# Optimization experiments

Hardware: AMD Instinct MI355X
Metric: run time of the kernel (lower is better)

The kernel has to match this reference:

```python
import jax, jax.numpy as jnp
import numpy as np

N_HEADS = 16
LN_EPS = 1e-6


def _mha(q_in, kv_in, mask, wq, bq, wk, bk, wv, bv, wo, bo):
    B, Sq, D = q_in.shape
    H = N_HEADS
    dh = D // H
    def split(x):  # [B,S,D] -> [B,H,S,dh]
        return x.reshape(B, -1, H, dh).transpose(0, 2, 1, 3)
    q = split(q_in @ wq + bq)
    k = split(kv_in @ wk + bk)
    v = split(kv_in @ wv + bv)
    scores = jnp.einsum('bhqd,bhkd->bhqk', q, k) / jnp.sqrt(jnp.asarray(dh, q.dtype))
    scores = scores + mask * (-1e9)
    attn = jax.nn.softmax(scores, axis=-1)
    out = jnp.einsum('bhqk,bhkd->bhqd', attn, v)
    out = out.transpose(0, 2, 1, 3).reshape(B, Sq, D)
    return out @ wo + bo


def _layer_norm(x, gamma, beta):
    mu = jnp.mean(x, axis=-1, keepdims=True)
    var = jnp.mean(jnp.square(x - mu), axis=-1, keepdims=True)
    return (x - mu) * jax.lax.rsqrt(var + LN_EPS) * gamma + beta


def setup_inputs() -> dict:
    key = jax.random.key(0)
    B, S_dec, S_enc, D, F = 4, 1024, 1024, 1024, 4096
    ks = jax.random.split(key, 16)
    s = 0.02
    inp = {
        'inputs': jax.random.normal(ks[0], (B, S_dec, D), jnp.float32),
        'enc_outputs': jax.random.normal(ks[1], (B, S_enc, D), jnp.float32),
        # causal look-ahead mask: 1 above diagonal -> -1e9 added to scores
        'mask_1': jnp.triu(jnp.ones((S_dec, S_dec), jnp.float32), k=1)[None, None],
        'mask_2': jnp.zeros((B, 1, 1, S_enc), jnp.float32),
    }
    names = ['wq1', 'wk1', 'wv1', 'wo1', 'wq2', 'wk2', 'wv2', 'wo2']
    for i, n in enumerate(names):
        inp[n] = jax.random.normal(ks[2 + i], (D, D), jnp.float32) * s
        inp['b' + n[1:]] = jnp.zeros((D,), jnp.float32)
    inp['w_ff1'] = jax.random.normal(ks[10], (D, F), jnp.float32) * s
    inp['b_ff1'] = jnp.zeros((F,), jnp.float32)
    inp['w_ff2'] = jax.random.normal(ks[11], (F, D), jnp.float32) * s
    inp['b_ff2'] = jnp.zeros((D,), jnp.float32)
    for i in (1, 2, 3):
        inp[f'g{i}'] = jnp.ones((D,), jnp.float32)
        inp[f'beta{i}'] = jnp.zeros((D,), jnp.float32)
    return inp


def reference(inputs, enc_outputs, mask_1, mask_2,
              wq1, bq1, wk1, bk1, wv1, bv1, wo1, bo1,
              wq2, bq2, wk2, bk2, wv2, bv2, wo2, bo2,
              w_ff1, b_ff1, w_ff2, b_ff2,
              g1, beta1, g2, beta2, g3, beta3):
    # causal self-attention + residual + LN (dropout inactive at inference)
    attn = _mha(inputs, inputs, mask_1, wq1, bq1, wk1, bk1, wv1, bv1, wo1, bo1)
    attn = _layer_norm(attn + inputs, g1, beta1)
    # encoder-decoder cross-attention + residual + LN
    attn2 = _mha(attn, enc_outputs, mask_2, wq2, bq2, wk2, bk2, wv2, bv2, wo2, bo2)
    attn2 = _layer_norm(attn2 + attn, g2, beta2)
    # FFN + residual + LN
    h = jax.nn.relu(attn2 @ w_ff1 + b_ff1)
    h = h @ w_ff2 + b_ff2
    return _layer_norm(h + attn2, g3, beta3)
```

## Files before the change

### kernel.cpp

```cpp
#include <hip/hip_runtime.h>
#include <stdint.h>

typedef unsigned short ushort_t;
typedef __attribute__((ext_vector_type(8))) short bf16x8;
typedef __attribute__((ext_vector_type(4))) float f32x4;
typedef __attribute__((ext_vector_type(4))) unsigned short us4;

#define DEV __device__ __forceinline__

DEV unsigned short f2bf(float f) {
  union { float f; unsigned u; } x; x.f = f;
  unsigned r = x.u + 0x7fffu + ((x.u >> 16) & 1u);
  return (unsigned short)(r >> 16);
}

DEV float bf2f(unsigned short u) {
  union { unsigned u; float f; } x; x.u = (unsigned)u << 16; return x.f;
}

DEV uint2 pk4(float v0, float v1, float v2, float v3) {
  unsigned d0, d1;
  asm("v_cvt_pk_bf16_f32 %0, %1, %2" : "=v"(d0) : "v"(v0), "v"(v1));
  asm("v_cvt_pk_bf16_f32 %0, %1, %2" : "=v"(d1) : "v"(v2), "v"(v3));
  uint2 r; r.x = d0; r.y = d1; return r;
}

DEV void gload16(const void* g, void* l) {
  __builtin_amdgcn_global_load_lds(
      (const __attribute__((address_space(1))) unsigned int*)g,
      (__attribute__((address_space(3))) unsigned int*)l, 16, 0, 0);
}

#define MFMA16 __builtin_amdgcn_mfma_f32_16x16x32_bf16

__global__ __launch_bounds__(256) void cast2_bf16_kernel(
    const float* __restrict__ x0, ushort_t* __restrict__ y0,
    const float* __restrict__ x1, ushort_t* __restrict__ y1) {
  int blk = blockIdx.x;
  const float* x = (blk < 4096) ? x0 : x1;
  ushort_t* y = (blk < 4096) ? y0 : y1;
  int i = (blk & 4095) * 256 + threadIdx.x;
  float4 v = ((const float4*)x)[i];
  us4 o; o.x = f2bf(v.x); o.y = f2bf(v.y); o.z = f2bf(v.z); o.w = f2bf(v.w);
  ((us4*)y)[i] = o;
}

__global__ __launch_bounds__(256) void reduce_cast_kernel(
    const ushort_t* __restrict__ p0, const ushort_t* __restrict__ p1,
    ushort_t* __restrict__ y, int n4) {
  int i = blockIdx.x * 256 + threadIdx.x;
  if (i >= n4) return;
  us4 a = ((const us4*)p0)[i];
  us4 b = ((const us4*)p1)[i];
  us4 o;
  o.x = f2bf(bf2f(a.x) + bf2f(b.x));
  o.y = f2bf(bf2f(a.y) + bf2f(b.y));
  o.z = f2bf(bf2f(a.z) + bf2f(b.z));
  o.w = f2bf(bf2f(a.w) + bf2f(b.w));
  ((us4*)y)[i] = o;
}

__global__ __launch_bounds__(256) void transpose_cast_kernel(
    const float* __restrict__ W, ushort_t* __restrict__ dst, int K, int N) {
  __shared__ float tile[64][65];
  int n0 = blockIdx.x * 64, k0 = blockIdx.y * 64;
  int tid = threadIdx.x;
#pragma unroll
  for (int it = 0; it < 16; ++it) {
    int idx = it * 256 + tid; int r = idx >> 6, c = idx & 63;
    tile[r][c] = W[(size_t)(k0 + r) * N + n0 + c];
  }
  __syncthreads();
#pragma unroll
  for (int it = 0; it < 16; ++it) {
    int idx = it * 256 + tid; int r = idx >> 6, c = idx & 63;
    dst[(size_t)(n0 + r) * K + k0 + c] = f2bf(tile[c][r]);
  }
}

struct Src8 { const float* p[8]; };
__global__ __launch_bounds__(256) void transpose_cast8_kernel(
    Src8 s, ushort_t* __restrict__ dst) {
  __shared__ float tile[64][65];
  const float* W = s.p[blockIdx.z];
  ushort_t* out = dst + (size_t)blockIdx.z * 1048576;
  int n0 = blockIdx.x * 64, k0 = blockIdx.y * 64;
  int tid = threadIdx.x;
#pragma unroll
  for (int it = 0; it < 16; ++it) {
    int idx = it * 256 + tid; int r = idx >> 6, c = idx & 63;
    tile[r][c] = W[(size_t)(k0 + r) * 1024 + n0 + c];
  }
  __syncthreads();
#pragma unroll
  for (int it = 0; it < 16; ++it) {
    int idx = it * 256 + tid; int r = idx >> 6, c = idx & 63;
    out[(size_t)(n0 + r) * 1024 + k0 + c] = f2bf(tile[c][r]);
  }
}

__global__ __launch_bounds__(256) void transpose_v_kernel(
    const ushort_t* __restrict__ V, int ldv, ushort_t* __restrict__ vT) {
  __shared__ ushort_t tile[64][65];
  int s0 = blockIdx.x * 64;
  int bh = blockIdx.y;
  int b = bh >> 4, h = bh & 15;
  int tid = threadIdx.x;
#pragma unroll
  for (int it = 0; it < 4; ++it) {
    int idx = it * 256 + tid; int r = idx >> 4, c = (idx & 15) * 4;
    us4 v = *(const us4*)&V[(size_t)(b * 1024 + s0 + r) * ldv + h * 64 + c];
    tile[r][c] = v.x; tile[r][c + 1] = v.y; tile[r][c + 2] = v.z; tile[r][c + 3] = v.w;
  }
  __syncthreads();
#pragma unroll
  for (int it = 0; it < 4; ++it) {
    int idx = it * 256 + tid; int r = idx >> 4, c = (idx & 15) * 4;
    us4 o; o.x = tile[c][r]; o.y = tile[c + 1][r]; o.z = tile[c + 2][r]; o.w = tile[c + 3][r];
    *(us4*)&vT[((size_t)bh * 64 + r) * 1024 + s0 + c] = o;
  }
}

template <int RELU>
__global__ __launch_bounds__(256, 2) void gemm_bt(
    const ushort_t* __restrict__ A, const ushort_t* __restrict__ Bt,
    const float* __restrict__ b0, const float* __restrict__ b1,
    const float* __restrict__ b2, const float* __restrict__ b3,
    ushort_t* __restrict__ Cb, int M, int N, int K, int Ks, long long pstr) {
  __shared__ ushort_t sA[4096];
  __shared__ ushort_t sB[4096];
  const int tid = threadIdx.x;
  const int w = tid >> 6, lane = tid & 63;
  const int lrow = lane & 15, lk = lane >> 4;
  const int m0 = blockIdx.x * 128, n0 = blockIdx.y * 128;
  const int kz = blockIdx.z * Ks;
  const int wr = w >> 1, wc = w & 1;
  f32x4 acc[4][4] = {};
  const int brow0 = (w * 1024 + lane * 16) >> 6;
  const int kbyte = (lane * 16) & 63;

  for (int kt = kz; kt < kz + Ks; kt += 32) {
    __syncthreads();
    const ushort_t* ga = A + (size_t)(m0 + brow0) * K + kt + (kbyte >> 1);
    gload16(ga, (char*)sA + w * 1024);
    gload16(ga + (size_t)64 * K, (char*)sA + 4096 + w * 1024);
    const ushort_t* gb = Bt + (size_t)(n0 + brow0) * K + kt + (kbyte >> 1);
    gload16(gb, (char*)sB + w * 1024);
    gload16(gb + (size_t)64 * K, (char*)sB + 4096 + w * 1024);
    __syncthreads();
    bf16x8 aF[4], bF[4];
#pragma unroll
    for (int t = 0; t < 4; ++t) {
      bF[t] = *(const bf16x8*)((const char*)sB + ((wc * 64 + t * 16 + lrow) << 6) + (lk << 4));
      aF[t] = *(const bf16x8*)((const char*)sA + ((wr * 64 + t * 16 + lrow) << 6) + (lk << 4));
    }
#pragma unroll
    for (int mt = 0; mt < 4; ++mt)
#pragma unroll
      for (int nt = 0; nt < 4; ++nt)
        acc[mt][nt] = MFMA16(bF[nt], aF[mt], acc[mt][nt], 0, 0, 0);
  }
  ushort_t* Cbz = Cb + (long long)blockIdx.z * pstr;
#pragma unroll
  for (int nt = 0; nt < 4; ++nt) {
    int colb = n0 + wc * 64 + nt * 16 + lk * 4;
    int seg = colb >> 10;
    const float* bp = seg == 0 ? b0 : seg == 1 ? b1 : seg == 2 ? b2 : b3;
    float4 bv = *(const float4*)(bp + (colb & 1023));
    if (blockIdx.z != 0) { bv.x = bv.y = bv.z = bv.w = 0.f; }
#pragma unroll
    for (int mt = 0; mt < 4; ++mt) {
      int row = m0 + wr * 64 + mt * 16 + lrow;
      float v0 = acc[mt][nt][0] + bv.x, v1 = acc[mt][nt][1] + bv.y;
      float v2 = acc[mt][nt][2] + bv.z, v3 = acc[mt][nt][3] + bv.w;
      if (RELU) {
        v0 = fmaxf(v0, 0.f); v1 = fmaxf(v1, 0.f);
        v2 = fmaxf(v2, 0.f); v3 = fmaxf(v3, 0.f);
      }
      *(uint2*)&Cbz[(size_t)row * N + colb] = pk4(v0, v1, v2, v3);
    }
  }
}

template <int RELU>
__global__ __launch_bounds__(512, 1) void gemm256(
    const ushort_t* __restrict__ A, const ushort_t* __restrict__ Bt,
    const float* __restrict__ b0, const float* __restrict__ b1,
    const float* __restrict__ b2, const float* __restrict__ b3,
    ushort_t* __restrict__ Cb, int M, int N, int K, int Ks, long long pstr) {
  extern __shared__ char L[];
  const int tid = threadIdx.x;
  const int w = tid >> 6, lane = tid & 63;
  const int lrow = lane & 15, lk = lane >> 4;
  const int wm = w >> 2, wn = w & 3;
  const int m0 = blockIdx.x * 256, n0 = blockIdx.y * 256;
  const int kz = blockIdx.z * Ks;
  const int nt = Ks >> 6;

  const int srow = w * 8 + (lane >> 3);
  const int gsw = (lane & 7) ^ ((lane >> 3) & 7);
  const ushort_t* srcA = A + (size_t)(m0 + srow) * K + kz + gsw * 8;
  const ushort_t* srcB = Bt + (size_t)(n0 + srow) * K + kz + gsw * 8;
  const int dstw = w * 1024;

#define STG4(M_, T_)                                                  \
  do {                                                                \
    const ushort_t* g0 = ((M_) ? srcB : srcA) + (size_t)(T_) * 64;    \
    char* d_ = L + (((T_) & 1) << 16) + ((M_) << 15) + dstw;          \
    gload16(g0, d_);                                                  \
    gload16(g0 + (size_t)64 * K, d_ + 8192);                          \
    gload16(g0 + (size_t)128 * K, d_ + 16384);                        \
    gload16(g0 + (size_t)192 * K, d_ + 24576);                        \
  } while (0)

  f32x4 acc[8][4] = {};
  const int swz = (lrow & 7) << 4;
  const int k0b = (lk << 4) ^ swz;
  const int k1b = (64 + (lk << 4)) ^ swz;
  const int aBase = (wm * 128 + lrow) << 7;
  const int bBase = ((wn * 64 + lrow) << 7) + 32768;

  STG4(0, 0); STG4(1, 0);
  asm volatile("s_waitcnt vmcnt(0)" ::: "memory");
  __builtin_amdgcn_s_barrier();

  for (int t = 0; t < nt; ++t) {
    const char* base = L + ((t & 1) << 16);
    bf16x8 aF[8], bF[4];
    if (t + 1 < nt) STG4(1, t + 1);
#pragma unroll
    for (int n = 0; n < 4; ++n) bF[n] = *(const bf16x8*)(base + bBase + n * 2048 + k0b);
#pragma unroll
    for (int m = 0; m < 8; ++m) aF[m] = *(const bf16x8*)(base + aBase + m * 2048 + k0b);
    __builtin_amdgcn_s_setprio(1);
#pragma unroll
    for (int m = 0; m < 8; ++m)
#pragma unroll
      for (int n = 0; n < 4; ++n)
        acc[m][n] = MFMA16(bF[n], aF[m], acc[m][n], 0, 0, 0);
    __builtin_amdgcn_s_setprio(0);
    if (t + 1 < nt) STG4(0, t + 1);
#pragma unroll
    for (int n = 0; n < 4; ++n) bF[n] = *(const bf16x8*)(base + bBase + n * 2048 + k1b);
#pragma unroll
    for (int m = 0; m < 8; ++m) aF[m] = *(const bf16x8*)(base + aBase + m * 2048 + k1b);
    __builtin_amdgcn_s_setprio(1);
#pragma unroll
    for (int m = 0; m < 8; ++m)
#pragma unroll
      for (int n = 0; n < 4; ++n)
        acc[m][n] = MFMA16(bF[n], aF[m], acc[m][n], 0, 0, 0);
    __builtin_amdgcn_s_setprio(0);
    asm volatile("s_waitcnt lgkmcnt(0)" ::: "memory");
    asm volatile("s_waitcnt vmcnt(0)" ::: "memory");
    __builtin_amdgcn_s_barrier();
  }
#undef STG4

  ushort_t* Cbz = Cb + (long long)blockIdx.z * pstr;
#pragma unroll
  for (int n = 0; n < 4; ++n) {
    int colb = n0 + wn * 64 + n * 16 + lk * 4;
    int seg = colb >> 10;
    const float* bp = seg == 0 ? b0 : seg == 1 ? b1 : seg == 2 ? b2 : b3;
    float4 bv = *(const float4*)(bp + (colb & 1023));
    if (blockIdx.z != 0) { bv.x = bv.y = bv.z = bv.w = 0.f; }
#pragma unroll
    for (int m = 0; m < 8; ++m) {
      int row = m0 + wm * 128 + m * 16 + lrow;
      float v0 = acc[m][n][0] + bv.x, v1 = acc[m][n][1] + bv.y;
      float v2 = acc[m][n][2] + bv.z, v3 = acc[m][n][3] + bv.w;
      if (RELU) {
        v0 = fmaxf(v0, 0.f); v1 = fmaxf(v1, 0.f);
        v2 = fmaxf(v2, 0.f); v3 = fmaxf(v3, 0.f);
      }
      *(uint2*)&Cbz[(size_t)row * N + colb] = pk4(v0, v1, v2, v3);
    }
  }
}

template <int CAUSAL>
__global__ __launch_bounds__(256, 3) void attn_kernel(
    const ushort_t* __restrict__ Q, int ldq,
    const ushort_t* __restrict__ Kp, int ldk,
    const ushort_t* __restrict__ vT,
    const float* __restrict__ mask2,
    ushort_t* __restrict__ O) {
  __shared__ ushort_t sK[2][4096];
  __shared__ ushort_t sV[2][4096];
  __shared__ ushort_t sP[4][2048];
  const int bh = blockIdx.x;
  const int yb = blockIdx.y;
  const int qb = (yb < 4) ? yb : 11 - yb;
  const int b = bh >> 4, h = bh & 15;
  const int tid = threadIdx.x, w = tid >> 6, lane = tid & 63;
  const int lrow = lane & 15, lk = lane >> 4;
  const int q0 = qb * 128 + w * 32;

  bf16x8 qF[2][2];
#pragma unroll
  for (int g = 0; g < 2; ++g) {
    const ushort_t* qptr =
        Q + (size_t)(b * 1024 + q0 + g * 16 + lrow) * ldq + h * 64 + lk * 8;
    qF[g][0] = *(const bf16x8*)qptr;
    qF[g][1] = *(const bf16x8*)(qptr + 32);
  }
  f32x4 oacc[2][4] = {};
  float m_[2] = {-3.0e38f, -3.0e38f}, l_[2] = {0.f, 0.f};
  const int nkb = CAUSAL ? (qb * 2 + 2) : 16;
  const float C = 0.18033688011112042f;

  const int sr = w * 16 + (lane >> 3);
  const int scb = (((lane & 7) ^ (lane >> 3)) * 16);
  const ushort_t* kbase = Kp + (size_t)(b * 1024 + sr) * ldk + h * 64 + (scb >> 1);
  const ushort_t* vbase = vT + ((size_t)bh * 64 + sr) * 1024 + (scb >> 1);
  char* dstK0 = (char*)sK[0] + w * 2048;
  char* dstV0 = (char*)sV[0] + w * 2048;

#define STAGE(kb_, bufi)                                              \
  do {                                                                \
    const ushort_t* gk = kbase + (size_t)(kb_) * 64 * ldk;            \
    gload16(gk, dstK0 + (bufi) * 8192);                               \
    gload16(gk + (size_t)8 * ldk, dstK0 + (bufi) * 8192 + 1024);      \
    const ushort_t* gv = vbase + (kb_) * 64;                          \
    gload16(gv, dstV0 + (bufi) * 8192);                               \
    gload16(gv + (size_t)8 * 1024, dstV0 + (bufi) * 8192 + 1024);     \
  } while (0)

  STAGE(0, 0);
  const int swz = (lrow & 7) << 4;

  for (int kb = 0; kb < nkb; ++kb) {
    const int buf = kb & 1;
    __syncthreads();
    if (kb + 1 < nkb) STAGE(kb + 1, buf ^ 1);

    const char* kB = (const char*)sK[buf];
    const char* vB = (const char*)sV[buf];
    bool skip[2], edge[2];
#pragma unroll
    for (int g = 0; g < 2; ++g) {
      int qming = q0 + g * 16;
      skip[g] = CAUSAL && (kb * 64 > qming + 15);
      edge[g] = CAUSAL && !skip[g] && (kb * 64 + 63 > qming);
    }
    f32x4 sc[2][4];
    __builtin_amdgcn_s_setprio(1);
#pragma unroll
    for (int kt = 0; kt < 4; ++kt) {
      const char* rp = kB + ((kt * 16 + lrow) << 7);
      bf16x8 k0 = *(const bf16x8*)(rp + ((lk * 16) ^ swz));
      bf16x8 k1 = *(const bf16x8*)(rp + ((64 + lk * 16) ^ swz));
      f32x4 z0 = {};
      z0 = MFMA16(k0, qF[0][0], z0, 0, 0, 0);
      sc[0][kt] = MFMA16(k1, qF[0][1], z0, 0, 0, 0);
      f32x4 z1 = {};
      z1 = MFMA16(k0, qF[1][0], z1, 0, 0, 0);
      sc[1][kt] = MFMA16(k1, qF[1][1], z1, 0, 0, 0);
    }
    __builtin_amdgcn_s_setprio(0);
    float4 mv[4];
    if (!CAUSAL) {
#pragma unroll
      for (int kt = 0; kt < 4; ++kt)
        mv[kt] = *(const float4*)&mask2[b * 1024 + kb * 64 + kt * 16 + lk * 4];
    }
#pragma unroll
    for (int g = 0; g < 2; ++g) {
      if (skip[g]) continue;
      if (CAUSAL) {
        if (edge[g]) {
          int qrel = q0 + g * 16 + lrow - kb * 64;
#pragma unroll
          for (int kt = 0; kt < 4; ++kt)
#pragma unroll
            for (int j = 0; j < 4; ++j)
              if (kt * 16 + lk * 4 + j > qrel) sc[g][kt][j] = -3.0e38f;
        }
      } else {
#pragma unroll
        for (int kt = 0; kt < 4; ++kt) {
          sc[g][kt][0] = fmaf(mv[kt].x, -8e9f, sc[g][kt][0]);
          sc[g][kt][1] = fmaf(mv[kt].y, -8e9f, sc[g][kt][1]);
          sc[g][kt][2] = fmaf(mv[kt].z, -8e9f, sc[g][kt][2]);
          sc[g][kt][3] = fmaf(mv[kt].w, -8e9f, sc[g][kt][3]);
        }
      }
      float a0 = fmaxf(fmaxf(sc[g][0][0], sc[g][0][1]), sc[g][0][2]);
      float a1 = fmaxf(fmaxf(sc[g][0][3], sc[g][1][0]), sc[g][1][1]);
      float a2 = fmaxf(fmaxf(sc[g][1][2], sc[g][1][3]), sc[g][2][0]);
      float a3 = fmaxf(fmaxf(sc[g][2][1], sc[g][2][2]), sc[g][2][3]);
      float a4 = fmaxf(fmaxf(sc[g][3][0], sc[g][3][1]), sc[g][3][2]);
      float pmax = fmaxf(fmaxf(fmaxf(a0, a1), fmaxf(a2, a3)),
                         fmaxf(a4, sc[g][3][3]));
      pmax = fmaxf(pmax, __shfl_xor(pmax, 16));
      pmax = fmaxf(pmax, __shfl_xor(pmax, 32));
      if (__any(pmax - m_[g] > 64.f)) {
        float mnew = fmaxf(m_[g], pmax);
        float scale = __builtin_exp2f((m_[g] - mnew) * C);
        l_[g] *= scale;
        m_[g] = mnew;
#pragma unroll
        for (int t = 0; t < 4; ++t) {
          oacc[g][t][0] *= scale; oacc[g][t][1] *= scale;
          oacc[g][t][2] *= scale; oacc[g][t][3] *= scale;
        }
      }
      const float mC = m_[g] * C;
      float psk[4] = {0.f, 0.f, 0.f, 0.f};
#pragma unroll
      for (int kt = 0; kt < 4; ++kt)
#pragma unroll
        for (int j = 0; j < 4; ++j) {
          float e = __builtin_exp2f(fmaf(sc[g][kt][j], C, -mC));
          sc[g][kt][j] = e;
          psk[kt] += e;
        }
      float ps = (psk[0] + psk[1]) + (psk[2] + psk[3]);
      ps += __shfl_xor(ps, 16);
      ps += __shfl_xor(ps, 32);
      l_[g] += ps;
      char* bp = (char*)sP[w] + (g * 16 + lrow) * 128;
#pragma unroll
      for (int kt = 0; kt < 4; ++kt) {
        uint2 dd = pk4(sc[g][kt][0], sc[g][kt][1], sc[g][kt][2], sc[g][kt][3]);
        *(uint2*)(bp + ((kt * 32 + lk * 8) ^ swz)) = dd;
      }
    }
    bf16x8 pF[2][2];
#pragma unroll
    for (int g = 0; g < 2; ++g) {
      if (skip[g]) continue;
      const char* pB = (const char*)sP[w] + (g * 16 + lrow) * 128;
      pF[g][0] = *(const bf16x8*)(pB + ((lk * 16) ^ swz));
      pF[g][1] = *(const bf16x8*)(pB + ((64 + lk * 16) ^ swz));
    }
    __builtin_amdgcn_s_setprio(1);
#pragma unroll
    for (int t = 0; t < 4; ++t) {
      const char* rp = vB + ((t * 16 + lrow) << 7);
      bf16x8 v0 = *(const bf16x8*)(rp + ((lk * 16) ^ swz));
      bf16x8 v1 = *(const bf16x8*)(rp + ((64 + lk * 16) ^ swz));
      if (!skip[0]) {
        oacc[0][t] = MFMA16(v0, pF[0][0], oacc[0][t], 0, 0, 0);
        oacc[0][t] = MFMA16(v1, pF[0][1], oacc[0][t], 0, 0, 0);
      }
      if (!skip[1]) {
        oacc[1][t] = MFMA16(v0, pF[1][0], oacc[1][t], 0, 0, 0);
        oacc[1][t] = MFMA16(v1, pF[1][1], oacc[1][t], 0, 0, 0);
      }
    }
    __builtin_amdgcn_s_setprio(0);
  }
#undef STAGE
#pragma unroll
  for (int g = 0; g < 2; ++g) {
    float invl = 1.f / l_[g];
    int row = q0 + g * 16 + lrow;
    ushort_t* op = O + (size_t)(b * 1024 + row) * 1024 + h * 64;
#pragma unroll
    for (int t = 0; t < 4; ++t) {
      uint2 dd = pk4(oacc[g][t][0] * invl, oacc[g][t][1] * invl,
                     oacc[g][t][2] * invl, oacc[g][t][3] * invl);
      *(uint2*)&op[t * 16 + lk * 4] = dd;
    }
  }
}

template <int RESBF, int NPART, int WF32>
__global__ __launch_bounds__(256) void ln_kernel(
    const ushort_t* __restrict__ p0, const ushort_t* __restrict__ p1,
    const ushort_t* __restrict__ p2, const ushort_t* __restrict__ p3,
    const void* __restrict__ rp,
    const float* __restrict__ g, const float* __restrict__ be,
    float* __restrict__ yf, ushort_t* __restrict__ yb) {
  int row = blockIdx.x, tid = threadIdx.x;
  size_t off = (size_t)row * 1024 + tid * 4;
  us4 a = *(const us4*)(p0 + off);
  float x0 = bf2f(a.x), x1 = bf2f(a.y), x2 = bf2f(a.z), x3 = bf2f(a.w);
  if (NPART >= 2) {
    us4 t = *(const us4*)(p1 + off);
    x0 += bf2f(t.x); x1 += bf2f(t.y); x2 += bf2f(t.z); x3 += bf2f(t.w);
  }
  if (NPART >= 4) {
    us4 t2 = *(const us4*)(p2 + off);
    us4 t3 = *(const us4*)(p3 + off);
    x0 += bf2f(t2.x) + bf2f(t3.x); x1 += bf2f(t2.y) + bf2f(t3.y);
    x2 += bf2f(t2.z) + bf2f(t3.z); x3 += bf2f(t2.w) + bf2f(t3.w);
  }
  if (RESBF) {
    us4 r = *(const us4*)((const ushort_t*)rp + off);
    x0 += bf2f(r.x); x1 += bf2f(r.y); x2 += bf2f(r.z); x3 += bf2f(r.w);
  } else {
    float4 r = *(const float4*)((const float*)rp + off);
    x0 += r.x; x1 += r.y; x2 += r.z; x3 += r.w;
  }
  float s = x0 + x1 + x2 + x3;
  float s2 = x0 * x0 + x1 * x1 + x2 * x2 + x3 * x3;
#pragma unroll
  for (int o = 1; o < 64; o <<= 1) { s += __shfl_xor(s, o); s2 += __shfl_xor(s2, o); }
  __shared__ float sh[8];
  if ((tid & 63) == 0) { sh[tid >> 6] = s; sh[4 + (tid >> 6)] = s2; }
  __syncthreads();
  s = sh[0] + sh[1] + sh[2] + sh[3];
  s2 = sh[4] + sh[5] + sh[6] + sh[7];
  float mu = s * 0.0009765625f;
  float var = s2 * 0.0009765625f - mu * mu;
  float inv = rsqrtf(var + 1e-6f);
  float4 gv = *(const float4*)(g + tid * 4);
  float4 bv = *(const float4*)(be + tid * 4);
  float y0 = (x0 - mu) * inv * gv.x + bv.x;
  float y1 = (x1 - mu) * inv * gv.y + bv.y;
  float y2 = (x2 - mu) * inv * gv.z + bv.z;
  float y3 = (x3 - mu) * inv * gv.w + bv.w;
  if (WF32) {
    *(float4*)(yf + off) = make_float4(y0, y1, y2, y3);
  } else {
    us4 o; o.x = f2bf(y0); o.y = f2bf(y1); o.z = f2bf(y2); o.w = f2bf(y3);
    *(us4*)(yb + off) = o;
  }
}

extern "C" void kernel_launch(void* const* d_in, const int* in_sizes, int n_in,
                              void* d_out, int out_size, void* d_ws, size_t ws_size,
                              hipStream_t stream) {
  (void)in_sizes; (void)n_in; (void)out_size; (void)ws_size;
  const float* inputs = (const float*)d_in[0];
  const float* enc    = (const float*)d_in[1];
  const float* mask2  = (const float*)d_in[3];
  const float* wq1 = (const float*)d_in[4];  const float* bq1 = (const float*)d_in[5];
  const float* wk1 = (const float*)d_in[6];  const float* bk1 = (const float*)d_in[7];
  const float* wv1 = (const float*)d_in[8];  const float* bv1 = (const float*)d_in[9];
  const float* wo1 = (const float*)d_in[10]; const float* bo1 = (const float*)d_in[11];
  const float* wq2 = (const float*)d_in[12]; const float* bq2 = (const float*)d_in[13];
  const float* wk2 = (const float*)d_in[14]; const float* bk2 = (const float*)d_in[15];
  const float* wv2 = (const float*)d_in[16]; const float* bv2 = (const float*)d_in[17];
  const float* wo2 = (const float*)d_in[18]; const float* bo2 = (const float*)d_in[19];
  const float* wff1 = (const float*)d_in[20]; const float* bff1 = (const float*)d_in[21];
  const float* wff2 = (const float*)d_in[22]; const float* bff2 = (const float*)d_in[23];
  const float* g1 = (const float*)d_in[24]; const float* be1 = (const float*)d_in[25];
  const float* g2 = (const float*)d_in[26]; const float* be2 = (const float*)d_in[27];
  const float* g3 = (const float*)d_in[28]; const float* be3 = (const float*)d_in[29];

  char* ws = (char*)d_ws;
  const size_t MB = 1024 * 1024;
  const size_t W1M = 1048576;
  ushort_t* wt    = (ushort_t*)ws;
  ushort_t* xb    = (ushort_t*)(ws + 32 * MB);
  ushort_t* encb  = (ushort_t*)(ws + 40 * MB);
  ushort_t* qkvb  = (ushort_t*)(ws + 48 * MB);
  ushort_t* vtb   = (ushort_t*)(ws + 72 * MB);
  ushort_t* attnb = (ushort_t*)(ws + 80 * MB);
  ushort_t* y1b   = (ushort_t*)(ws + 88 * MB);
  ushort_t* y2b   = (ushort_t*)(ws + 96 * MB);
  ushort_t* cp    = (ushort_t*)(ws + 104 * MB);
  ushort_t* q2b   = (ushort_t*)(ws + 32 * MB);
  ushort_t* kv2b  = (ushort_t*)(ws + 56 * MB);
  ushort_t* hb    = (ushort_t*)(ws + 32 * MB);
  ushort_t* pp    = (ushort_t*)(ws + 104 * MB);
  float* outf = (float*)d_out;
  const long long PE = 4LL * 1024 * 1024;

  cast2_bf16_kernel<<<8192, 256, 0, stream>>>(inputs, xb, enc, encb);
  Src8 s8; s8.p[0] = wq1; s8.p[1] = wk1; s8.p[2] = wv1; s8.p[3] = wo1;
           s8.p[4] = wq2; s8.p[5] = wk2; s8.p[6] = wv2; s8.p[7] = wo2;
  transpose_cast8_kernel<<<dim3(16, 16, 8), 256, 0, stream>>>(s8, wt);
  transpose_cast_kernel<<<dim3(64, 16), 256, 0, stream>>>(wff1, wt + 8 * W1M, 1024, 4096);
  transpose_cast_kernel<<<dim3(16, 64), 256, 0, stream>>>(wff2, wt + 12 * W1M, 4096, 1024);

  gemm256<0><<<dim3(16, 12, 1), 512, 131072, stream>>>(
      xb, wt, bq1, bk1, bv1, bv1, qkvb, 4096, 3072, 1024, 1024, 0);
  transpose_v_kernel<<<dim3(16, 64), 256, 0, stream>>>(qkvb + 2048, 3072, vtb);
  attn_kernel<1><<<dim3(64, 8), 256, 0, stream>>>(
      qkvb, 3072, qkvb + 1024, 3072, vtb, nullptr, attnb);
  gemm_bt<0><<<dim3(32, 8, 2), 256, 0, stream>>>(
      attnb, wt + 3 * W1M, bo1, bo1, bo1, bo1, cp, 4096, 1024, 1024, 512, PE);
  ln_kernel<0, 2, 0><<<4096, 256, 0, stream>>>(cp, cp + PE, nullptr, nullptr,
                                               inputs, g1, be1, nullptr, y1b);

  gemm_bt<0><<<dim3(32, 8, 2), 256, 0, stream>>>(
      y1b, wt + 4 * W1M, bq2, bq2, bq2, bq2, cp, 4096, 1024, 1024, 512, PE);
  reduce_cast_kernel<<<4096, 256, 0, stream>>>(cp, cp + PE, q2b, 1048576);
  gemm_bt<0><<<dim3(32, 16, 1), 256, 0, stream>>>(
      encb, wt + 5 * W1M, bk2, bv2, bk2, bk2, kv2b, 4096, 2048, 1024, 1024, 0);
  transpose_v_kernel<<<dim3(16, 64), 256, 0, stream>>>(kv2b + 1024, 2048, vtb);
  attn_kernel<0><<<dim3(64, 8), 256, 0, stream>>>(
      q2b, 1024, kv2b, 2048, vtb, mask2, attnb);
  gemm_bt<0><<<dim3(32, 8, 2), 256, 0, stream>>>(
      attnb, wt + 7 * W1M, bo2, bo2, bo2, bo2, cp, 4096, 1024, 1024, 512, PE);
  ln_kernel<1, 2, 0><<<4096, 256, 0, stream>>>(cp, cp + PE, nullptr, nullptr,
                                               y1b, g2, be2, nullptr, y2b);

  gemm256<1><<<dim3(16, 16, 1), 512, 131072, stream>>>(
      y2b, wt + 8 * W1M, bff1, bff1 + 1024, bff1 + 2048, bff1 + 3072,
      hb, 4096, 4096, 1024, 1024, 0);
  gemm256<0><<<dim3(16, 4, 4), 512, 131072, stream>>>(
      hb, wt + 12 * W1M, bff2, bff2, bff2, bff2, pp, 4096, 1024, 4096, 1024, PE);
  ln_kernel<1, 4, 1><<<4096, 256, 0, stream>>>(pp, pp + PE, pp + 2 * PE, pp + 3 * PE,
                                               y2b, g3, be3, outf, nullptr);
}
```

Baseline: 347.0 us.

## Split attention KV range across two blocks and merge with combine kernel

```diff
diff --git a/kernel.cpp b/kernel.cpp
--- a/kernel.cpp
+++ b/kernel.cpp
@@ -280,18 +280,20 @@
 }
 
 template <int CAUSAL>
-__global__ __launch_bounds__(256, 3) void attn_kernel(
+__global__ __launch_bounds__(256, 4) void attn_kernel(
     const ushort_t* __restrict__ Q, int ldq,
     const ushort_t* __restrict__ Kp, int ldk,
     const ushort_t* __restrict__ vT,
     const float* __restrict__ mask2,
-    ushort_t* __restrict__ O) {
+    ushort_t* __restrict__ op,
+    float2* __restrict__ ml) {
   __shared__ ushort_t sK[2][4096];
   __shared__ ushort_t sV[2][4096];
-  __shared__ ushort_t sP[4][2048];
+  __shared__ ushort_t sP[4][1024];
   const int bh = blockIdx.x;
   const int yb = blockIdx.y;
   const int qb = (yb < 4) ? yb : 11 - yb;
+  const int hz = blockIdx.z;
   const int b = bh >> 4, h = bh & 15;
   const int tid = threadIdx.x, w = tid >> 6, lane = tid & 63;
   const int lrow = lane & 15, lk = lane >> 4;
@@ -307,7 +309,10 @@
   }
   f32x4 oacc[2][4] = {};
   float m_[2] = {-3.0e38f, -3.0e38f}, l_[2] = {0.f, 0.f};
-  const int nkb = CAUSAL ? (qb * 2 + 2) : 16;
+  const int ntile = CAUSAL ? (qb * 2 + 2) : 16;
+  const int half0 = (ntile + 1) >> 1;
+  const int tLo = hz ? half0 : 0;
+  const int tHi = hz ? ntile : half0;
   const float C = 0.18033688011112042f;
 
   const int sr = w * 16 + (lane >> 3);
@@ -327,13 +332,13 @@
     gload16(gv + (size_t)8 * 1024, dstV0 + (bufi) * 8192 + 1024);     \
   } while (0)
 
-  STAGE(0, 0);
+  STAGE(tLo, 0);
   const int swz = (lrow & 7) << 4;
 
-  for (int kb = 0; kb < nkb; ++kb) {
-    const int buf = kb & 1;
+  for (int kb = tLo; kb < tHi; ++kb) {
+    const int buf = (kb - tLo) & 1;
     __syncthreads();
-    if (kb + 1 < nkb) STAGE(kb + 1, buf ^ 1);
+    if (kb + 1 < tHi) STAGE(kb + 1, buf ^ 1);
 
     const char* kB = (const char*)sK[buf];
     const char* vB = (const char*)sV[buf];
@@ -344,6 +349,7 @@
       skip[g] = CAUSAL && (kb * 64 > qming + 15);
       edge[g] = CAUSAL && !skip[g] && (kb * 64 + 63 > qming);
     }
+    if (CAUSAL && skip[0] && skip[1]) continue;
     f32x4 sc[2][4];
     __builtin_amdgcn_s_setprio(1);
 #pragma unroll
@@ -365,6 +371,7 @@
       for (int kt = 0; kt < 4; ++kt)
         mv[kt] = *(const float4*)&mask2[b * 1024 + kb * 64 + kt * 16 + lk * 4];
     }
+    bf16x8 pF[2][2];
 #pragma unroll
     for (int g = 0; g < 2; ++g) {
       if (skip[g]) continue;
@@ -420,20 +427,14 @@
       ps += __shfl_xor(ps, 16);
       ps += __shfl_xor(ps, 32);
       l_[g] += ps;
-      char* bp = (char*)sP[w] + (g * 16 + lrow) * 128;
+      char* bp = (char*)sP[w] + lrow * 128;
 #pragma unroll
       for (int kt = 0; kt < 4; ++kt) {
         uint2 dd = pk4(sc[g][kt][0], sc[g][kt][1], sc[g][kt][2], sc[g][kt][3]);
         *(uint2*)(bp + ((kt * 32 + lk * 8) ^ swz)) = dd;
       }
-    }
-    bf16x8 pF[2][2];
-#pragma unroll
-    for (int g = 0; g < 2; ++g) {
-      if (skip[g]) continue;
-      const char* pB = (const char*)sP[w] + (g * 16 + lrow) * 128;
-      pF[g][0] = *(const bf16x8*)(pB + ((lk * 16) ^ swz));
-      pF[g][1] = *(const bf16x8*)(pB + ((64 + lk * 16) ^ swz));
+      pF[g][0] = *(const bf16x8*)(bp + ((lk * 16) ^ swz));
+      pF[g][1] = *(const bf16x8*)(bp + ((64 + lk * 16) ^ swz));
     }
     __builtin_amdgcn_s_setprio(1);
 #pragma unroll
@@ -455,16 +456,49 @@
 #undef STAGE
 #pragma unroll
   for (int g = 0; g < 2; ++g) {
-    float invl = 1.f / l_[g];
     int row = q0 + g * 16 + lrow;
-    ushort_t* op = O + (size_t)(b * 1024 + row) * 1024 + h * 64;
+    size_t rbase = (size_t)bh * 1024 + row;
+    if (lk == 0) {
+      float2 v; v.x = m_[g]; v.y = l_[g];
+      ml[(size_t)hz * 65536 + rbase] = v;
+    }
+    ushort_t* opp = op + (size_t)hz * 4194304 + rbase * 64;
 #pragma unroll
     for (int t = 0; t < 4; ++t) {
-      uint2 dd = pk4(oacc[g][t][0] * invl, oacc[g][t][1] * invl,
-                     oacc[g][t][2] * invl, oacc[g][t][3] * invl);
-      *(uint2*)&op[t * 16 + lk * 4] = dd;
-    }
-  }
+      uint2 dd = pk4(oacc[g][t][0], oacc[g][t][1], oacc[g][t][2], oacc[g][t][3]);
+      *(uint2*)&opp[t * 16 + lk * 4] = dd;
+    }
+  }
+}
+
+__global__ __launch_bounds__(256) void attn_combine_kernel(
+    const ushort_t* __restrict__ op, const float2* __restrict__ ml,
+    ushort_t* __restrict__ O) {
+  const int r = blockIdx.x;
+  const int b = r >> 10, row = r & 1023;
+  const int tid = threadIdx.x;
+  __shared__ float s0s[16], s1s[16], ivs[16];
+  if (tid < 16) {
+    size_t rb = (size_t)(b * 16 + tid) * 1024 + row;
+    float2 a = ml[rb];
+    float2 c = ml[65536 + rb];
+    float m = fmaxf(a.x, c.x);
+    float e0 = __builtin_exp2f((a.x - m) * 0.18033688011112042f);
+    float e1 = __builtin_exp2f((c.x - m) * 0.18033688011112042f);
+    s0s[tid] = e0; s1s[tid] = e1;
+    ivs[tid] = 1.f / (e0 * a.y + e1 * c.y);
+  }
+  __syncthreads();
+  const int h = tid >> 4, d = (tid & 15) * 4;
+  size_t base = ((size_t)(b * 16 + h) * 1024 + row) * 64 + d;
+  us4 a4 = *(const us4*)&op[base];
+  us4 b4 = *(const us4*)&op[4194304 + base];
+  float s0 = s0s[h], s1 = s1s[h], iv = ivs[h];
+  float o0 = (bf2f(a4.x) * s0 + bf2f(b4.x) * s1) * iv;
+  float o1 = (bf2f(a4.y) * s0 + bf2f(b4.y) * s1) * iv;
+  float o2 = (bf2f(a4.z) * s0 + bf2f(b4.z) * s1) * iv;
+  float o3 = (bf2f(a4.w) * s0 + bf2f(b4.w) * s1) * iv;
+  *(uint2*)&O[(size_t)r * 1024 + h * 64 + d] = pk4(o0, o1, o2, o3);
 }
 
 template <int RESBF, int NPART, int WF32>
@@ -554,6 +588,8 @@
   ushort_t* y1b   = (ushort_t*)(ws + 88 * MB);
   ushort_t* y2b   = (ushort_t*)(ws + 96 * MB);
   ushort_t* cp    = (ushort_t*)(ws + 104 * MB);
+  ushort_t* opart = (ushort_t*)(ws + 104 * MB);
+  float2*   mlb   = (float2*)(ws + 136 * MB);
   ushort_t* q2b   = (ushort_t*)(ws + 32 * MB);
   ushort_t* kv2b  = (ushort_t*)(ws + 56 * MB);
   ushort_t* hb    = (ushort_t*)(ws + 32 * MB);
@@ -571,8 +607,9 @@
   gemm256<0><<<dim3(16, 12, 1), 512, 131072, stream>>>(
       xb, wt, bq1, bk1, bv1, bv1, qkvb, 4096, 3072, 1024, 1024, 0);
   transpose_v_kernel<<<dim3(16, 64), 256, 0, stream>>>(qkvb + 2048, 3072, vtb);
-  attn_kernel<1><<<dim3(64, 8), 256, 0, stream>>>(
-      qkvb, 3072, qkvb + 1024, 3072, vtb, nullptr, attnb);
+  attn_kernel<1><<<dim3(64, 8, 2), 256, 0, stream>>>(
+      qkvb, 3072, qkvb + 1024, 3072, vtb, nullptr, opart, mlb);
+  attn_combine_kernel<<<4096, 256, 0, stream>>>(opart, mlb, attnb);
   gemm_bt<0><<<dim3(32, 8, 2), 256, 0, stream>>>(
       attnb, wt + 3 * W1M, bo1, bo1, bo1, bo1, cp, 4096, 1024, 1024, 512, PE);
   ln_kernel<0, 2, 0><<<4096, 256, 0, stream>>>(cp, cp + PE, nullptr, nullptr,
@@ -584,8 +621,9 @@
   gemm_bt<0><<<dim3(32, 16, 1), 256, 0, stream>>>(
       encb, wt + 5 * W1M, bk2, bv2, bk2, bk2, kv2b, 4096, 2048, 1024, 1024, 0);
   transpose_v_kernel<<<dim3(16, 64), 256, 0, stream>>>(kv2b + 1024, 2048, vtb);
-  attn_kernel<0><<<dim3(64, 8), 256, 0, stream>>>(
-      q2b, 1024, kv2b, 2048, vtb, mask2, attnb);
+  attn_kernel<0><<<dim3(64, 8, 2), 256, 0, stream>>>(
+      q2b, 1024, kv2b, 2048, vtb, mask2, opart, mlb);
+  attn_combine_kernel<<<4096, 256, 0, stream>>>(opart, mlb, attnb);
   gemm_bt<0><<<dim3(32, 8, 2), 256, 0, stream>>>(
       attnb, wt + 7 * W1M, bo2, bo2, bo2, bo2, cp, 4096, 1024, 1024, 512, PE);
   ln_kernel<1, 2, 0><<<4096, 256, 0, stream>>>(cp, cp + PE, nullptr, nullptr,
```

Result: slower. 360.5 us (+3.9%).
